# Kernel tuning notes

Measured on AMD Instinct MI355X. Metric: run time of the kernel, lower is better.

## Reference

```python
import jax, jax.numpy as jnp
import numpy as np

ROPE_BASE = 10000.0


def _rope_cos_sin(seq_len, head_dim, dtype=jnp.float32):
    theta = 1.0 / (ROPE_BASE ** (jnp.arange(0, head_dim, 2, dtype=jnp.float32) / head_dim))
    angles = jnp.arange(seq_len, dtype=jnp.float32)[:, None] * theta[None, :]  # [S, hd/2]
    return jnp.cos(angles).astype(dtype), jnp.sin(angles).astype(dtype)


def _apply_rope(x, cos, sin):
    # x: [B, H, S, hd]; cos/sin: [S, hd/2] broadcast over B,H (interleaved pairing)
    x1 = x[..., 0::2]
    x2 = x[..., 1::2]
    c = cos[None, None, :, :]
    s = sin[None, None, :, :]
    y1 = x1 * c - x2 * s
    y2 = x1 * s + x2 * c
    return jnp.stack([y1, y2], axis=-1).reshape(x.shape)


def setup_inputs() -> dict:
    key = jax.random.key(0)
    ks = jax.random.split(key, 5)
    B, S, D = 2, 2048, 1024
    std = 1.0 / np.sqrt(D)
    return {
        "x": jax.random.normal(ks[0], (B, S, D), dtype=jnp.float32),
        "Wq": jax.random.normal(ks[1], (D, D), dtype=jnp.float32) * std,
        "Wk": jax.random.normal(ks[2], (D, D), dtype=jnp.float32) * std,
        "Wv": jax.random.normal(ks[3], (D, D), dtype=jnp.float32) * std,
        "Wo": jax.random.normal(ks[4], (D, D), dtype=jnp.float32) * std,
        "n_heads": 16,
    }


def reference(x, Wq, Wk, Wv, Wo, n_heads):
    B, S, D = x.shape
    H = n_heads
    hd = D // H
    # QKV projections (nn.Linear: x @ W.T), split into heads -> [B, H, S, hd]
    def proj(W):
        return (x @ W.T).reshape(B, S, H, hd).transpose(0, 2, 1, 3)
    q, k, v = proj(Wq), proj(Wk), proj(Wv)
    cos, sin = _rope_cos_sin(S, hd, x.dtype)
    q = _apply_rope(q, cos, sin)
    k = _apply_rope(k, cos, sin)
    # causal scaled dot-product attention
    scale = 1.0 / np.sqrt(hd)
    scores = jnp.einsum('bhqd,bhkd->bhqk', q, k) * scale
    causal = jnp.tril(jnp.ones((S, S), dtype=bool))
    scores = jnp.where(causal[None, None], scores, jnp.finfo(scores.dtype).min)
    attn = jax.nn.softmax(scores, axis=-1)
    out = jnp.einsum('bhqk,bhkd->bhqd', attn, v)  # [B,H,S,hd]
    out = out.transpose(0, 2, 1, 3).reshape(B, S, D)
    return out @ Wo.T
```

## Files before the change

### kernel.cpp

```cpp
#include <hip/hip_runtime.h>
#include <stdint.h>

#define B_  2
#define S_  2048
#define D_  1024
#define H_  16
#define HD_ 64
#define M_  (B_ * S_)
#define XN_ ((size_t)M_ * D_)
#define WN_ ((size_t)D_ * D_)

using bf16x8 = __attribute__((ext_vector_type(8))) short;
using f32x4  = __attribute__((ext_vector_type(4))) float;

__device__ __forceinline__ unsigned short f2bf(float f) {
    union { float f; unsigned u; } v; v.f = f;
    unsigned u = v.u;
    return (unsigned short)((u + 0x7fffu + ((u >> 16) & 1u)) >> 16);
}
__device__ __forceinline__ unsigned short f2bf_trunc(float f) {
    union { float f; unsigned u; } v; v.f = f;
    return (unsigned short)(v.u >> 16);
}
__device__ __forceinline__ float bf2f(unsigned short s) {
    union { unsigned u; float f; } v; v.u = ((unsigned)s) << 16;
    return v.f;
}

__device__ __forceinline__ void gload_lds16(const unsigned short* g, unsigned short* l) {
    __builtin_amdgcn_global_load_lds((const __attribute__((address_space(1))) void*)g,
                                     (__attribute__((address_space(3))) void*)l, 16, 0, 0);
}

__global__ __launch_bounds__(256) void cvt_kernel(
    const float* __restrict__ x,
    const float* __restrict__ Wq, const float* __restrict__ Wk,
    const float* __restrict__ Wv, const float* __restrict__ Wo,
    unsigned short* __restrict__ xb,
    unsigned short* __restrict__ Wqb, unsigned short* __restrict__ Wkb,
    unsigned short* __restrict__ Wvb, unsigned short* __restrict__ Wob)
{
    size_t i = ((size_t)blockIdx.x * 256 + threadIdx.x) * 8;
    const float* src; unsigned short* dst; size_t off;
    if (i < XN_) { src = x; dst = xb; off = i; }
    else {
        size_t j = i - XN_;
        int w = (int)(j >> 20);
        off = j & (WN_ - 1);
        src = (w == 0) ? Wq : (w == 1) ? Wk : (w == 2) ? Wv : Wo;
        dst = (w == 0) ? Wqb : (w == 1) ? Wkb : (w == 2) ? Wvb : Wob;
    }
    float4 a = *(const float4*)(src + off);
    float4 b = *(const float4*)(src + off + 4);
    bf16x8 o;
    o[0] = (short)f2bf(a.x); o[1] = (short)f2bf(a.y);
    o[2] = (short)f2bf(a.z); o[3] = (short)f2bf(a.w);
    o[4] = (short)f2bf(b.x); o[5] = (short)f2bf(b.y);
    o[6] = (short)f2bf(b.z); o[7] = (short)f2bf(b.w);
    *(bf16x8*)(dst + off) = o;
}

__global__ __launch_bounds__(256, 3) void qkv_rope_kernel(
    const unsigned short* __restrict__ x,
    const unsigned short* __restrict__ Wq,
    const unsigned short* __restrict__ Wk,
    const unsigned short* __restrict__ Wv,
    unsigned short* __restrict__ Qo,
    unsigned short* __restrict__ Ko,
    unsigned short* __restrict__ Vt)
{
    __shared__ unsigned short As[128 * 64];
    __shared__ unsigned short Bs[128 * 64];
    const int which = blockIdx.z;
    const unsigned short* __restrict__ W = (which == 0) ? Wq : (which == 1) ? Wk : Wv;
    const int tid  = threadIdx.x;
    const int lane = tid & 63, wave = tid >> 6;
    const int col  = lane & 15, quad = lane >> 4;
    const int wm = (wave >> 1) * 64, wn = (wave & 1) * 64;
    const int n0 = blockIdx.x * 128, m0 = blockIdx.y * 128;
    const int sr = tid >> 3;
    const int sc = tid & 7;
    const int ssw = ((sc ^ (sr & 7)) * 8);

    f32x4 acc[4][4];
#pragma unroll
    for (int i = 0; i < 4; ++i)
#pragma unroll
        for (int j = 0; j < 4; ++j) acc[i][j] = (f32x4){0.f, 0.f, 0.f, 0.f};

    for (int k0 = 0; k0 < D_; k0 += 64) {
        __syncthreads();
#pragma unroll
        for (int g = 0; g < 4; ++g) {
            gload_lds16(x + (size_t)(m0 + g * 32 + sr) * D_ + k0 + ssw, As + g * 2048 + tid * 8);
            gload_lds16(W + (size_t)(n0 + g * 32 + sr) * D_ + k0 + ssw, Bs + g * 2048 + tid * 8);
        }
        __syncthreads();
#pragma unroll
        for (int kk = 0; kk < 2; ++kk) {
            bf16x8 af[4], bf[4];
#pragma unroll
            for (int i = 0; i < 4; ++i) {
                const int R = wm + i * 16 + col;
                af[i] = *(const bf16x8*)&As[R * 64 + (((kk * 4 + quad) ^ (R & 7)) * 8)];
            }
#pragma unroll
            for (int j = 0; j < 4; ++j) {
                const int R = wn + j * 16 + col;
                bf[j] = *(const bf16x8*)&Bs[R * 64 + (((kk * 4 + quad) ^ (R & 7)) * 8)];
            }
#pragma unroll
            for (int i = 0; i < 4; ++i)
#pragma unroll
                for (int j = 0; j < 4; ++j)
                    acc[i][j] = __builtin_amdgcn_mfma_f32_16x16x32_bf16(af[i], bf[j], acc[i][j], 0, 0, 0);
        }
    }

#pragma unroll
    for (int i = 0; i < 4; ++i) {
        const int mg0    = m0 + wm + i * 16 + quad * 4;
        const int bb     = mg0 >> 11;
        const int s_base = mg0 & (S_ - 1);
#pragma unroll
        for (int j = 0; j < 4; ++j) {
            const int n  = n0 + wn + j * 16 + col;
            const int h  = n >> 6;
            const int dd = n & 63;
            if (which < 2) {
                unsigned short* __restrict__ O = (which == 0) ? Qo : Ko;
                const float theta  = __expf(-0.2878231366242557f * (float)(dd >> 1));
                const float qscale = (which == 0) ? 0.125f : 1.0f;
#pragma unroll
                for (int r = 0; r < 4; ++r) {
                    float v  = acc[i][j][r];
                    float vp = __shfl_xor(v, 1);
                    float ang = theta * (float)(s_base + r);
                    float sn, cs; __sincosf(ang, &sn, &cs);
                    float y = (dd & 1) ? (vp * sn + v * cs) : (v * cs - vp * sn);
                    O[((size_t)(bb * H_ + h) * S_ + s_base + r) * HD_ + dd] = f2bf(y * qscale);
                }
            } else {
                ushort4 pk;
                pk.x = f2bf(acc[i][j][0]); pk.y = f2bf(acc[i][j][1]);
                pk.z = f2bf(acc[i][j][2]); pk.w = f2bf(acc[i][j][3]);
                *(ushort4*)(Vt + ((size_t)(bb * H_ + h) * HD_ + dd) * S_ + s_base) = pk;
            }
        }
    }
}

#define PST 72

__global__ __launch_bounds__(256, 3) void attn_kernel(
    const unsigned short* __restrict__ Q,
    const unsigned short* __restrict__ K,
    const unsigned short* __restrict__ Vt,
    unsigned short* __restrict__ num0,
    unsigned short* __restrict__ num1,
    float* __restrict__ den0,
    float* __restrict__ den1)
{
    __shared__ unsigned short KS[64 * 64];
    __shared__ unsigned short VS[64 * 64];
    __shared__ unsigned short Plds[4][16 * PST];
    const int tid  = threadIdx.x;
    const int lane = tid & 63;
    const int wave = tid >> 6;
    const int col  = lane & 15;
    const int quad = lane >> 4;
    const int id = blockIdx.x;
    const int bh = (id & 7) * 4 + ((id >> 3) & 3);
    const int ph = id >> 5;
    const int p  = ph & 7;
    const int hf = ph >> 3;
    const int b = bh >> 4, h = bh & 15;

    unsigned short* __restrict__ nout = hf ? num1 : num0;
    float*          __restrict__ dout = hf ? den1 : den0;

    const unsigned short* Qb = Q  + (size_t)bh * S_ * HD_;
    const unsigned short* Kb = K  + (size_t)bh * S_ * HD_;
    const unsigned short* Vb = Vt + (size_t)bh * HD_ * S_;

    const int srow = tid >> 3;
    const int schk = tid & 7;
    const int ssw0 = (schk ^ (srow & 7)) * 8;

    bf16x8 vone;
#pragma unroll
    for (int e = 0; e < 8; ++e) vone[e] = (short)0x3F80;
    const f32x4 z4 = (f32x4){0.f, 0.f, 0.f, 0.f};
    const float MFIX = 12.0f;

    for (int tt = 0; tt < 2; ++tt) {
        const int t_ = tt ? (15 - p) : p;
        const int q0blk = t_ * 128;
        const int q0w   = q0blk + wave * 32;
        const int nsteps = (q0blk + 128) >> 6;

        bf16x8 aq[2][2];
#pragma unroll
        for (int st = 0; st < 2; ++st) {
            aq[st][0] = *(const bf16x8*)(Qb + (size_t)(q0w + st * 16 + col) * HD_ + quad * 8);
            aq[st][1] = *(const bf16x8*)(Qb + (size_t)(q0w + st * 16 + col) * HD_ + 32 + quad * 8);
        }
        f32x4 acc[2][5];
#pragma unroll
        for (int st = 0; st < 2; ++st)
#pragma unroll
            for (int t = 0; t < 5; ++t) acc[st][t] = (f32x4){0.f, 0.f, 0.f, 0.f};

        for (int s = hf; s < nsteps; s += 2) {
            const int j0 = s << 6;
            __syncthreads();
            gload_lds16(Kb + (size_t)(j0 + srow) * HD_ + ssw0,      KS + tid * 8);
            gload_lds16(Kb + (size_t)(j0 + srow + 32) * HD_ + ssw0, KS + 2048 + tid * 8);
            gload_lds16(Vb + (size_t)srow * S_ + j0 + ssw0,         VS + tid * 8);
            gload_lds16(Vb + (size_t)(srow + 32) * S_ + j0 + ssw0,  VS + 2048 + tid * 8);
            __syncthreads();

            f32x4 sc[2][4];
#pragma unroll
            for (int t2 = 0; t2 < 4; ++t2) {
                const int kr = t2 * 16 + col;
                bf16x8 k0 = *(const bf16x8*)&KS[kr * 64 + ((quad ^ (kr & 7)) * 8)];
                bf16x8 k1 = *(const bf16x8*)&KS[kr * 64 + (((4 + quad) ^ (kr & 7)) * 8)];
                sc[0][t2] = __builtin_amdgcn_mfma_f32_16x16x32_bf16(aq[0][0], k0, z4, 0, 0, 0);
                sc[0][t2] = __builtin_amdgcn_mfma_f32_16x16x32_bf16(aq[0][1], k1, sc[0][t2], 0, 0, 0);
                sc[1][t2] = __builtin_amdgcn_mfma_f32_16x16x32_bf16(aq[1][0], k0, z4, 0, 0, 0);
                sc[1][t2] = __builtin_amdgcn_mfma_f32_16x16x32_bf16(aq[1][1], k1, sc[1][t2], 0, 0, 0);
            }
            bf16x8 vf[8];
#pragma unroll
            for (int t = 0; t < 4; ++t) {
                const int dr = t * 16 + col;
                vf[t * 2]     = *(const bf16x8*)&VS[dr * 64 + ((quad ^ (dr & 7)) * 8)];
                vf[t * 2 + 1] = *(const bf16x8*)&VS[dr * 64 + (((4 + quad) ^ (dr & 7)) * 8)];
            }

#pragma unroll
            for (int st = 0; st < 2; ++st) {
                const bool need_mask = (j0 + 63 > q0w + st * 16);
#pragma unroll
                for (int r = 0; r < 4; ++r) {
                    const int qrow = q0w + st * 16 + quad * 4 + r;
                    float v0 = sc[st][0][r], v1 = sc[st][1][r], v2 = sc[st][2][r], v3 = sc[st][3][r];
                    if (need_mask) {
                        if (j0 + col      > qrow) v0 = -1.0e38f;
                        if (j0 + 16 + col > qrow) v1 = -1.0e38f;
                        if (j0 + 32 + col > qrow) v2 = -1.0e38f;
                        if (j0 + 48 + col > qrow) v3 = -1.0e38f;
                    }
                    const int rb = (quad * 4 + r) * PST;
                    Plds[wave][rb + col]      = f2bf_trunc(__expf(v0 - MFIX));
                    Plds[wave][rb + 16 + col] = f2bf_trunc(__expf(v1 - MFIX));
                    Plds[wave][rb + 32 + col] = f2bf_trunc(__expf(v2 - MFIX));
                    Plds[wave][rb + 48 + col] = f2bf_trunc(__expf(v3 - MFIX));
                }
                bf16x8 ap0 = *(const bf16x8*)&Plds[wave][col * PST + quad * 8];
                bf16x8 ap1 = *(const bf16x8*)&Plds[wave][col * PST + 32 + quad * 8];
#pragma unroll
                for (int t = 0; t < 4; ++t) {
                    acc[st][t] = __builtin_amdgcn_mfma_f32_16x16x32_bf16(ap0, vf[t * 2], acc[st][t], 0, 0, 0);
                    acc[st][t] = __builtin_amdgcn_mfma_f32_16x16x32_bf16(ap1, vf[t * 2 + 1], acc[st][t], 0, 0, 0);
                }
                acc[st][4] = __builtin_amdgcn_mfma_f32_16x16x32_bf16(ap0, vone, acc[st][4], 0, 0, 0);
                acc[st][4] = __builtin_amdgcn_mfma_f32_16x16x32_bf16(ap1, vone, acc[st][4], 0, 0, 0);
            }
        }

#pragma unroll
        for (int st = 0; st < 2; ++st) {
#pragma unroll
            for (int t = 0; t < 4; ++t)
#pragma unroll
                for (int r = 0; r < 4; ++r) {
                    const int qrow = q0w + st * 16 + quad * 4 + r;
                    nout[(size_t)(b * S_ + qrow) * D_ + h * HD_ + t * 16 + col] =
                        f2bf(acc[st][t][r]);
                }
            if (col == 0) {
#pragma unroll
                for (int r = 0; r < 4; ++r) {
                    const int qrow = q0w + st * 16 + quad * 4 + r;
                    dout[(size_t)(b * S_ + qrow) * H_ + h] = acc[st][4][r];
                }
            }
        }
    }
}

__global__ __launch_bounds__(256) void combine_kernel(
    const unsigned short* __restrict__ num0,
    unsigned short* __restrict__ A,
    const float* __restrict__ den0,
    const float* __restrict__ den1)
{
    size_t idx = ((size_t)blockIdx.x * 256 + threadIdx.x) * 8;
    size_t row = idx >> 10;
    int hh = (int)((idx >> 6) & 15);
    float inv = 1.0f / (den0[row * H_ + hh] + den1[row * H_ + hh]);
    bf16x8 a = *(const bf16x8*)(num0 + idx);
    bf16x8 c = *(const bf16x8*)(A + idx);
    bf16x8 o;
#pragma unroll
    for (int e = 0; e < 8; ++e)
        o[e] = (short)f2bf((bf2f((unsigned short)a[e]) + bf2f((unsigned short)c[e])) * inv);
    *(bf16x8*)(A + idx) = o;
}

__global__ __launch_bounds__(256, 3) void oproj_kernel(
    const unsigned short* __restrict__ A,
    const unsigned short* __restrict__ Wo,
    float* __restrict__ out)
{
    __shared__ unsigned short As[128 * 64];
    __shared__ unsigned short Bs[128 * 64];
    const int tid  = threadIdx.x;
    const int lane = tid & 63, wave = tid >> 6;
    const int col  = lane & 15, quad = lane >> 4;
    const int wm = (wave >> 1) * 64, wn = (wave & 1) * 64;
    const int n0 = blockIdx.x * 128, m0 = blockIdx.y * 128;
    const int sr = tid >> 3;
    const int sc = tid & 7;
    const int ssw = ((sc ^ (sr & 7)) * 8);

    f32x4 acc[4][4];
#pragma unroll
    for (int i = 0; i < 4; ++i)
#pragma unroll
        for (int j = 0; j < 4; ++j) acc[i][j] = (f32x4){0.f, 0.f, 0.f, 0.f};

    for (int k0 = 0; k0 < D_; k0 += 64) {
        __syncthreads();
#pragma unroll
        for (int g = 0; g < 4; ++g) {
            gload_lds16(A  + (size_t)(m0 + g * 32 + sr) * D_ + k0 + ssw, As + g * 2048 + tid * 8);
            gload_lds16(Wo + (size_t)(n0 + g * 32 + sr) * D_ + k0 + ssw, Bs + g * 2048 + tid * 8);
        }
        __syncthreads();
#pragma unroll
        for (int kk = 0; kk < 2; ++kk) {
            bf16x8 af[4], bf[4];
#pragma unroll
            for (int i = 0; i < 4; ++i) {
                const int R = wm + i * 16 + col;
                af[i] = *(const bf16x8*)&As[R * 64 + (((kk * 4 + quad) ^ (R & 7)) * 8)];
            }
#pragma unroll
            for (int j = 0; j < 4; ++j) {
                const int R = wn + j * 16 + col;
                bf[j] = *(const bf16x8*)&Bs[R * 64 + (((kk * 4 + quad) ^ (R & 7)) * 8)];
            }
#pragma unroll
            for (int i = 0; i < 4; ++i)
#pragma unroll
                for (int j = 0; j < 4; ++j)
                    acc[i][j] = __builtin_amdgcn_mfma_f32_16x16x32_bf16(af[i], bf[j], acc[i][j], 0, 0, 0);
        }
    }
#pragma unroll
    for (int i = 0; i < 4; ++i) {
        const int mg0 = m0 + wm + i * 16 + quad * 4;
#pragma unroll
        for (int j = 0; j < 4; ++j) {
            const int n = n0 + wn + j * 16 + col;
#pragma unroll
            for (int r = 0; r < 4; ++r)
                out[(size_t)(mg0 + r) * D_ + n] = acc[i][j][r];
        }
    }
}

extern "C" void kernel_launch(void* const* d_in, const int* in_sizes, int n_in,
                              void* d_out, int out_size, void* d_ws, size_t ws_size,
                              hipStream_t stream)
{
    const float* x  = (const float*)d_in[0];
    const float* Wq = (const float*)d_in[1];
    const float* Wk = (const float*)d_in[2];
    const float* Wv = (const float*)d_in[3];
    const float* Wo = (const float*)d_in[4];

    unsigned short* xb  = (unsigned short*)d_ws;
    unsigned short* Wqb = xb  + XN_;
    unsigned short* Wkb = Wqb + WN_;
    unsigned short* Wvb = Wkb + WN_;
    unsigned short* Wob = Wvb + WN_;
    unsigned short* Qw  = Wob + WN_;
    unsigned short* Kw  = Qw  + XN_;
    unsigned short* Vtw = Kw  + XN_;
    unsigned short* Aw  = Vtw + XN_;

    unsigned short* num0 = xb;
    float*          den0 = (float*)Wqb;
    float*          den1 = den0 + (size_t)M_ * H_;

    const int cvt_blocks = (int)((XN_ + 4 * WN_) / (8 * 256));
    cvt_kernel<<<cvt_blocks, 256, 0, stream>>>(x, Wq, Wk, Wv, Wo, xb, Wqb, Wkb, Wvb, Wob);
    qkv_rope_kernel<<<dim3(D_ / 128, M_ / 128, 3), 256, 0, stream>>>(xb, Wqb, Wkb, Wvb, Qw, Kw, Vtw);
    attn_kernel<<<512, 256, 0, stream>>>(Qw, Kw, Vtw, num0, Aw, den0, den1);
    combine_kernel<<<(int)(XN_ / (8 * 256)), 256, 0, stream>>>(num0, Aw, den0, den1);
    oproj_kernel<<<dim3(D_ / 128, M_ / 128), 256, 0, stream>>>(Aw, Wob, (float*)d_out);
}
```

Baseline: 172.6 us.

## Double-buffer LDS tiles in QKV, attention and output projection kernels

Each GEMM kernel and the attention kernel now keeps two LDS buffers and issues the global-to-LDS loads for the next K tile before computing on the current one. This cuts the main loop to one barrier per iteration instead of two. The aim is to hide global load latency behind MFMA work. In exchange the GEMM kernels use twice the LDS, and their launch bounds drop from 3 to 2 blocks per CU.

```diff
diff --git a/kernel.cpp b/kernel.cpp
--- a/kernel.cpp
+++ b/kernel.cpp
@@ -60,7 +60,7 @@
     *(bf16x8*)(dst + off) = o;
 }
 
-__global__ __launch_bounds__(256, 3) void qkv_rope_kernel(
+__global__ __launch_bounds__(256, 2) void qkv_rope_kernel(
     const unsigned short* __restrict__ x,
     const unsigned short* __restrict__ Wq,
     const unsigned short* __restrict__ Wk,
@@ -69,8 +69,8 @@
     unsigned short* __restrict__ Ko,
     unsigned short* __restrict__ Vt)
 {
-    __shared__ unsigned short As[128 * 64];
-    __shared__ unsigned short Bs[128 * 64];
+    __shared__ unsigned short As[2][128 * 64];
+    __shared__ unsigned short Bs[2][128 * 64];
     const int which = blockIdx.z;
     const unsigned short* __restrict__ W = (which == 0) ? Wq : (which == 1) ? Wk : Wv;
     const int tid  = threadIdx.x;
@@ -82,32 +82,38 @@
     const int sc = tid & 7;
     const int ssw = ((sc ^ (sr & 7)) * 8);
 
+    auto stage = [&](int k0, int bsel) {
+#pragma unroll
+        for (int g = 0; g < 4; ++g) {
+            gload_lds16(x + (size_t)(m0 + g * 32 + sr) * D_ + k0 + ssw, &As[bsel][g * 2048 + tid * 8]);
+            gload_lds16(W + (size_t)(n0 + g * 32 + sr) * D_ + k0 + ssw, &Bs[bsel][g * 2048 + tid * 8]);
+        }
+    };
+
     f32x4 acc[4][4];
 #pragma unroll
     for (int i = 0; i < 4; ++i)
 #pragma unroll
         for (int j = 0; j < 4; ++j) acc[i][j] = (f32x4){0.f, 0.f, 0.f, 0.f};
 
-    for (int k0 = 0; k0 < D_; k0 += 64) {
+    stage(0, 0);
+    for (int it = 0; it < 16; ++it) {
         __syncthreads();
-#pragma unroll
-        for (int g = 0; g < 4; ++g) {
-            gload_lds16(x + (size_t)(m0 + g * 32 + sr) * D_ + k0 + ssw, As + g * 2048 + tid * 8);
-            gload_lds16(W + (size_t)(n0 + g * 32 + sr) * D_ + k0 + ssw, Bs + g * 2048 + tid * 8);
-        }
-        __syncthreads();
+        if (it + 1 < 16) stage((it + 1) * 64, (it + 1) & 1);
+        const unsigned short* Ab = &As[it & 1][0];
+        const unsigned short* Bb = &Bs[it & 1][0];
 #pragma unroll
         for (int kk = 0; kk < 2; ++kk) {
             bf16x8 af[4], bf[4];
 #pragma unroll
             for (int i = 0; i < 4; ++i) {
                 const int R = wm + i * 16 + col;
-                af[i] = *(const bf16x8*)&As[R * 64 + (((kk * 4 + quad) ^ (R & 7)) * 8)];
+                af[i] = *(const bf16x8*)&Ab[R * 64 + (((kk * 4 + quad) ^ (R & 7)) * 8)];
             }
 #pragma unroll
             for (int j = 0; j < 4; ++j) {
                 const int R = wn + j * 16 + col;
-                bf[j] = *(const bf16x8*)&Bs[R * 64 + (((kk * 4 + quad) ^ (R & 7)) * 8)];
+                bf[j] = *(const bf16x8*)&Bb[R * 64 + (((kk * 4 + quad) ^ (R & 7)) * 8)];
             }
 #pragma unroll
             for (int i = 0; i < 4; ++i)
@@ -161,8 +167,8 @@
     float* __restrict__ den0,
     float* __restrict__ den1)
 {
-    __shared__ unsigned short KS[64 * 64];
-    __shared__ unsigned short VS[64 * 64];
+    __shared__ unsigned short KS[2][64 * 64];
+    __shared__ unsigned short VS[2][64 * 64];
     __shared__ unsigned short Plds[4][16 * PST];
     const int tid  = threadIdx.x;
     const int lane = tid & 63;
@@ -187,6 +193,13 @@
     const int schk = tid & 7;
     const int ssw0 = (schk ^ (srow & 7)) * 8;
 
+    auto stageKV = [&](int j0, int bsel) {
+        gload_lds16(Kb + (size_t)(j0 + srow) * HD_ + ssw0,      &KS[bsel][tid * 8]);
+        gload_lds16(Kb + (size_t)(j0 + srow + 32) * HD_ + ssw0, &KS[bsel][2048 + tid * 8]);
+        gload_lds16(Vb + (size_t)srow * S_ + j0 + ssw0,         &VS[bsel][tid * 8]);
+        gload_lds16(Vb + (size_t)(srow + 32) * S_ + j0 + ssw0,  &VS[bsel][2048 + tid * 8]);
+    };
+
     bf16x8 vone;
 #pragma unroll
     for (int e = 0; e < 8; ++e) vone[e] = (short)0x3F80;
@@ -197,7 +210,7 @@
         const int t_ = tt ? (15 - p) : p;
         const int q0blk = t_ * 128;
         const int q0w   = q0blk + wave * 32;
-        const int nsteps = (q0blk + 128) >> 6;
+        const int scount = t_ + 1;
 
         bf16x8 aq[2][2];
 #pragma unroll
@@ -211,21 +224,21 @@
 #pragma unroll
             for (int t = 0; t < 5; ++t) acc[st][t] = (f32x4){0.f, 0.f, 0.f, 0.f};
 
-        for (int s = hf; s < nsteps; s += 2) {
-            const int j0 = s << 6;
+        __syncthreads();
+        stageKV(hf << 6, 0);
+        for (int si = 0; si < scount; ++si) {
+            const int j0 = (hf + 2 * si) << 6;
             __syncthreads();
-            gload_lds16(Kb + (size_t)(j0 + srow) * HD_ + ssw0,      KS + tid * 8);
-            gload_lds16(Kb + (size_t)(j0 + srow + 32) * HD_ + ssw0, KS + 2048 + tid * 8);
-            gload_lds16(Vb + (size_t)srow * S_ + j0 + ssw0,         VS + tid * 8);
-            gload_lds16(Vb + (size_t)(srow + 32) * S_ + j0 + ssw0,  VS + 2048 + tid * 8);
-            __syncthreads();
+            if (si + 1 < scount) stageKV((hf + 2 * (si + 1)) << 6, (si + 1) & 1);
+            const unsigned short* KSb = &KS[si & 1][0];
+            const unsigned short* VSb = &VS[si & 1][0];
 
             f32x4 sc[2][4];
 #pragma unroll
             for (int t2 = 0; t2 < 4; ++t2) {
                 const int kr = t2 * 16 + col;
-                bf16x8 k0 = *(const bf16x8*)&KS[kr * 64 + ((quad ^ (kr & 7)) * 8)];
-                bf16x8 k1 = *(const bf16x8*)&KS[kr * 64 + (((4 + quad) ^ (kr & 7)) * 8)];
+                bf16x8 k0 = *(const bf16x8*)&KSb[kr * 64 + ((quad ^ (kr & 7)) * 8)];
+                bf16x8 k1 = *(const bf16x8*)&KSb[kr * 64 + (((4 + quad) ^ (kr & 7)) * 8)];
                 sc[0][t2] = __builtin_amdgcn_mfma_f32_16x16x32_bf16(aq[0][0], k0, z4, 0, 0, 0);
                 sc[0][t2] = __builtin_amdgcn_mfma_f32_16x16x32_bf16(aq[0][1], k1, sc[0][t2], 0, 0, 0);
                 sc[1][t2] = __builtin_amdgcn_mfma_f32_16x16x32_bf16(aq[1][0], k0, z4, 0, 0, 0);
@@ -235,8 +248,8 @@
 #pragma unroll
             for (int t = 0; t < 4; ++t) {
                 const int dr = t * 16 + col;
-                vf[t * 2]     = *(const bf16x8*)&VS[dr * 64 + ((quad ^ (dr & 7)) * 8)];
-                vf[t * 2 + 1] = *(const bf16x8*)&VS[dr * 64 + (((4 + quad) ^ (dr & 7)) * 8)];
+                vf[t * 2]     = *(const bf16x8*)&VSb[dr * 64 + ((quad ^ (dr & 7)) * 8)];
+                vf[t * 2 + 1] = *(const bf16x8*)&VSb[dr * 64 + (((4 + quad) ^ (dr & 7)) * 8)];
             }
 
 #pragma unroll
@@ -310,13 +323,13 @@
     *(bf16x8*)(A + idx) = o;
 }
 
-__global__ __launch_bounds__(256, 3) void oproj_kernel(
+__global__ __launch_bounds__(256, 2) void oproj_kernel(
     const unsigned short* __restrict__ A,
     const unsigned short* __restrict__ Wo,
     float* __restrict__ out)
 {
-    __shared__ unsigned short As[128 * 64];
-    __shared__ unsigned short Bs[128 * 64];
+    __shared__ unsigned short As[2][128 * 64];
+    __shared__ unsigned short Bs[2][128 * 64];
     const int tid  = threadIdx.x;
     const int lane = tid & 63, wave = tid >> 6;
     const int col  = lane & 15, quad = lane >> 4;
@@ -326,32 +339,38 @@
     const int sc = tid & 7;
     const int ssw = ((sc ^ (sr & 7)) * 8);
 
+    auto stage = [&](int k0, int bsel) {
+#pragma unroll
+        for (int g = 0; g < 4; ++g) {
+            gload_lds16(A  + (size_t)(m0 + g * 32 + sr) * D_ + k0 + ssw, &As[bsel][g * 2048 + tid * 8]);
+            gload_lds16(Wo + (size_t)(n0 + g * 32 + sr) * D_ + k0 + ssw, &Bs[bsel][g * 2048 + tid * 8]);
+        }
+    };
+
     f32x4 acc[4][4];
 #pragma unroll
     for (int i = 0; i < 4; ++i)
 #pragma unroll
         for (int j = 0; j < 4; ++j) acc[i][j] = (f32x4){0.f, 0.f, 0.f, 0.f};
 
-    for (int k0 = 0; k0 < D_; k0 += 64) {
+    stage(0, 0);
+    for (int it = 0; it < 16; ++it) {
         __syncthreads();
-#pragma unroll
-        for (int g = 0; g < 4; ++g) {
-            gload_lds16(A  + (size_t)(m0 + g * 32 + sr) * D_ + k0 + ssw, As + g * 2048 + tid * 8);
-            gload_lds16(Wo + (size_t)(n0 + g * 32 + sr) * D_ + k0 + ssw, Bs + g * 2048 + tid * 8);
-        }
-        __syncthreads();
+        if (it + 1 < 16) stage((it + 1) * 64, (it + 1) & 1);
+        const unsigned short* Ab = &As[it & 1][0];
+        const unsigned short* Bb = &Bs[it & 1][0];
 #pragma unroll
         for (int kk = 0; kk < 2; ++kk) {
             bf16x8 af[4], bf[4];
 #pragma unroll
             for (int i = 0; i < 4; ++i) {
                 const int R = wm + i * 16 + col;
-                af[i] = *(const bf16x8*)&As[R * 64 + (((kk * 4 + quad) ^ (R & 7)) * 8)];
+                af[i] = *(const bf16x8*)&Ab[R * 64 + (((kk * 4 + quad) ^ (R & 7)) * 8)];
             }
 #pragma unroll
             for (int j = 0; j < 4; ++j) {
                 const int R = wn + j * 16 + col;
-                bf[j] = *(const bf16x8*)&Bs[R * 64 + (((kk * 4 + quad) ^ (R & 7)) * 8)];
+                bf[j] = *(const bf16x8*)&Bb[R * 64 + (((kk * 4 + quad) ^ (R & 7)) * 8)];
             }
 #pragma unroll
             for (int i = 0; i < 4; ++i)
```

Result: slower. 186.4 us (+8.0%).

## Double-buffer LDS tiles with BK=32 in QKV and output projection GEMMs

Applied to the files above, without the earlier changes.

Both projection GEMM kernels switch from a single 64-wide K tile with two barriers per step to two 32-wide K buffers in LDS. The next tile is prefetched into the other buffer while MFMAs run on the current one, using one barrier per iteration and a swizzle adjusted for 32-wide rows. The aim is to hide global-to-LDS load latency behind compute. The cost is twice as many loop iterations with half the MFMA work each. Correctness also depends on the async LDS loads having completed by the single barrier.

```diff
diff --git a/kernel.cpp b/kernel.cpp
--- a/kernel.cpp
+++ b/kernel.cpp
@@ -69,8 +69,8 @@
     unsigned short* __restrict__ Ko,
     unsigned short* __restrict__ Vt)
 {
-    __shared__ unsigned short As[128 * 64];
-    __shared__ unsigned short Bs[128 * 64];
+    __shared__ unsigned short As[2][128 * 32];
+    __shared__ unsigned short Bs[2][128 * 32];
     const int which = blockIdx.z;
     const unsigned short* __restrict__ W = (which == 0) ? Wq : (which == 1) ? Wk : Wv;
     const int tid  = threadIdx.x;
@@ -78,9 +78,17 @@
     const int col  = lane & 15, quad = lane >> 4;
     const int wm = (wave >> 1) * 64, wn = (wave & 1) * 64;
     const int n0 = blockIdx.x * 128, m0 = blockIdx.y * 128;
-    const int sr = tid >> 3;
-    const int sc = tid & 7;
-    const int ssw = ((sc ^ (sr & 7)) * 8);
+    const int sr = tid >> 2;
+    const int sc = tid & 3;
+    const int ssw = ((sc ^ (sr & 3)) * 8);
+
+    auto stage = [&](int k0, int bsel) {
+#pragma unroll
+        for (int g = 0; g < 2; ++g) {
+            gload_lds16(x + (size_t)(m0 + g * 64 + sr) * D_ + k0 + ssw, &As[bsel][g * 2048 + tid * 8]);
+            gload_lds16(W + (size_t)(n0 + g * 64 + sr) * D_ + k0 + ssw, &Bs[bsel][g * 2048 + tid * 8]);
+        }
+    };
 
     f32x4 acc[4][4];
 #pragma unroll
@@ -88,33 +96,28 @@
 #pragma unroll
         for (int j = 0; j < 4; ++j) acc[i][j] = (f32x4){0.f, 0.f, 0.f, 0.f};
 
-    for (int k0 = 0; k0 < D_; k0 += 64) {
+    stage(0, 0);
+    for (int it = 0; it < 32; ++it) {
         __syncthreads();
-#pragma unroll
-        for (int g = 0; g < 4; ++g) {
-            gload_lds16(x + (size_t)(m0 + g * 32 + sr) * D_ + k0 + ssw, As + g * 2048 + tid * 8);
-            gload_lds16(W + (size_t)(n0 + g * 32 + sr) * D_ + k0 + ssw, Bs + g * 2048 + tid * 8);
-        }
-        __syncthreads();
-#pragma unroll
-        for (int kk = 0; kk < 2; ++kk) {
-            bf16x8 af[4], bf[4];
-#pragma unroll
-            for (int i = 0; i < 4; ++i) {
-                const int R = wm + i * 16 + col;
-                af[i] = *(const bf16x8*)&As[R * 64 + (((kk * 4 + quad) ^ (R & 7)) * 8)];
-            }
-#pragma unroll
-            for (int j = 0; j < 4; ++j) {
-                const int R = wn + j * 16 + col;
-                bf[j] = *(const bf16x8*)&Bs[R * 64 + (((kk * 4 + quad) ^ (R & 7)) * 8)];
-            }
-#pragma unroll
-            for (int i = 0; i < 4; ++i)
-#pragma unroll
-                for (int j = 0; j < 4; ++j)
-                    acc[i][j] = __builtin_amdgcn_mfma_f32_16x16x32_bf16(af[i], bf[j], acc[i][j], 0, 0, 0);
-        }
+        if (it + 1 < 32) stage((it + 1) * 32, (it + 1) & 1);
+        const unsigned short* Ab = &As[it & 1][0];
+        const unsigned short* Bb = &Bs[it & 1][0];
+        bf16x8 af[4], bf[4];
+#pragma unroll
+        for (int i = 0; i < 4; ++i) {
+            const int R = wm + i * 16 + col;
+            af[i] = *(const bf16x8*)&Ab[R * 32 + ((quad ^ (R & 3)) * 8)];
+        }
+#pragma unroll
+        for (int j = 0; j < 4; ++j) {
+            const int R = wn + j * 16 + col;
+            bf[j] = *(const bf16x8*)&Bb[R * 32 + ((quad ^ (R & 3)) * 8)];
+        }
+#pragma unroll
+        for (int i = 0; i < 4; ++i)
+#pragma unroll
+            for (int j = 0; j < 4; ++j)
+                acc[i][j] = __builtin_amdgcn_mfma_f32_16x16x32_bf16(af[i], bf[j], acc[i][j], 0, 0, 0);
     }
 
 #pragma unroll
@@ -315,16 +318,24 @@
     const unsigned short* __restrict__ Wo,
     float* __restrict__ out)
 {
-    __shared__ unsigned short As[128 * 64];
-    __shared__ unsigned short Bs[128 * 64];
+    __shared__ unsigned short As[2][128 * 32];
+    __shared__ unsigned short Bs[2][128 * 32];
     const int tid  = threadIdx.x;
     const int lane = tid & 63, wave = tid >> 6;
     const int col  = lane & 15, quad = lane >> 4;
     const int wm = (wave >> 1) * 64, wn = (wave & 1) * 64;
     const int n0 = blockIdx.x * 128, m0 = blockIdx.y * 128;
-    const int sr = tid >> 3;
-    const int sc = tid & 7;
-    const int ssw = ((sc ^ (sr & 7)) * 8);
+    const int sr = tid >> 2;
+    const int sc = tid & 3;
+    const int ssw = ((sc ^ (sr & 3)) * 8);
+
+    auto stage = [&](int k0, int bsel) {
+#pragma unroll
+        for (int g = 0; g < 2; ++g) {
+            gload_lds16(A  + (size_t)(m0 + g * 64 + sr) * D_ + k0 + ssw, &As[bsel][g * 2048 + tid * 8]);
+            gload_lds16(Wo + (size_t)(n0 + g * 64 + sr) * D_ + k0 + ssw, &Bs[bsel][g * 2048 + tid * 8]);
+        }
+    };
 
     f32x4 acc[4][4];
 #pragma unroll
@@ -332,33 +343,28 @@
 #pragma unroll
         for (int j = 0; j < 4; ++j) acc[i][j] = (f32x4){0.f, 0.f, 0.f, 0.f};
 
-    for (int k0 = 0; k0 < D_; k0 += 64) {
+    stage(0, 0);
+    for (int it = 0; it < 32; ++it) {
         __syncthreads();
-#pragma unroll
-        for (int g = 0; g < 4; ++g) {
-            gload_lds16(A  + (size_t)(m0 + g * 32 + sr) * D_ + k0 + ssw, As + g * 2048 + tid * 8);
-            gload_lds16(Wo + (size_t)(n0 + g * 32 + sr) * D_ + k0 + ssw, Bs + g * 2048 + tid * 8);
-        }
-        __syncthreads();
-#pragma unroll
-        for (int kk = 0; kk < 2; ++kk) {
-            bf16x8 af[4], bf[4];
-#pragma unroll
-            for (int i = 0; i < 4; ++i) {
-                const int R = wm + i * 16 + col;
-                af[i] = *(const bf16x8*)&As[R * 64 + (((kk * 4 + quad) ^ (R & 7)) * 8)];
-            }
-#pragma unroll
-            for (int j = 0; j < 4; ++j) {
-                const int R = wn + j * 16 + col;
-                bf[j] = *(const bf16x8*)&Bs[R * 64 + (((kk * 4 + quad) ^ (R & 7)) * 8)];
-            }
-#pragma unroll
-            for (int i = 0; i < 4; ++i)
-#pragma unroll
-                for (int j = 0; j < 4; ++j)
-                    acc[i][j] = __builtin_amdgcn_mfma_f32_16x16x32_bf16(af[i], bf[j], acc[i][j], 0, 0, 0);
-        }
+        if (it + 1 < 32) stage((it + 1) * 32, (it + 1) & 1);
+        const unsigned short* Ab = &As[it & 1][0];
+        const unsigned short* Bb = &Bs[it & 1][0];
+        bf16x8 af[4], bf[4];
+#pragma unroll
+        for (int i = 0; i < 4; ++i) {
+            const int R = wm + i * 16 + col;
+            af[i] = *(const bf16x8*)&Ab[R * 32 + ((quad ^ (R & 3)) * 8)];
+        }
+#pragma unroll
+        for (int j = 0; j < 4; ++j) {
+            const int R = wn + j * 16 + col;
+            bf[j] = *(const bf16x8*)&Bb[R * 32 + ((quad ^ (R & 3)) * 8)];
+        }
+#pragma unroll
+        for (int i = 0; i < 4; ++i)
+#pragma unroll
+            for (int j = 0; j < 4; ++j)
+                acc[i][j] = __builtin_amdgcn_mfma_f32_16x16x32_bf16(af[i], bf[j], acc[i][j], 0, 0, 0);
     }
 #pragma unroll
     for (int i = 0; i < 4; ++i) {
```

Measured after the change: 181.1 us. 1.05x slower.

## Transpose attention MFMA operands to pack P writes and fold softmax constants

Applied to the files above, without the earlier changes.

Swaps the operand order of the QK^T and PV MFMAs so each lane holds four consecutive key scores for a single query. That lets the probability tile be written to LDS as one packed 8-byte store per tile instead of many scalar 2-byte stores, and lets the numerator be written to global memory as packed ushort4 stores. The log2(e) factor is folded into the Q scale and the fixed max offset into the MFMA accumulator init, so the softmax uses exp2f with no per-element subtract. The masking index math changes to match the transposed layout, and the denominator path stays in the original layout; getting either wrong would change results.

```diff
diff --git a/kernel.cpp b/kernel.cpp
--- a/kernel.cpp
+++ b/kernel.cpp
@@ -18,13 +18,12 @@
     unsigned u = v.u;
     return (unsigned short)((u + 0x7fffu + ((u >> 16) & 1u)) >> 16);
 }
-__device__ __forceinline__ unsigned short f2bf_trunc(float f) {
-    union { float f; unsigned u; } v; v.f = f;
-    return (unsigned short)(v.u >> 16);
-}
 __device__ __forceinline__ float bf2f(unsigned short s) {
     union { unsigned u; float f; } v; v.u = ((unsigned)s) << 16;
     return v.f;
+}
+__device__ __forceinline__ unsigned fbits(float f) {
+    union { float f; unsigned u; } v; v.f = f; return v.u;
 }
 
 __device__ __forceinline__ void gload_lds16(const unsigned short* g, unsigned short* l) {
@@ -130,7 +129,7 @@
             if (which < 2) {
                 unsigned short* __restrict__ O = (which == 0) ? Qo : Ko;
                 const float theta  = __expf(-0.2878231366242557f * (float)(dd >> 1));
-                const float qscale = (which == 0) ? 0.125f : 1.0f;
+                const float qscale = (which == 0) ? 0.18033688f : 1.0f;
 #pragma unroll
                 for (int r = 0; r < 4; ++r) {
                     float v  = acc[i][j][r];
@@ -151,6 +150,7 @@
 }
 
 #define PST 72
+#define MFIX2 17.312340490667561f
 
 __global__ __launch_bounds__(256, 3) void attn_kernel(
     const unsigned short* __restrict__ Q,
@@ -190,8 +190,7 @@
     bf16x8 vone;
 #pragma unroll
     for (int e = 0; e < 8; ++e) vone[e] = (short)0x3F80;
-    const f32x4 z4 = (f32x4){0.f, 0.f, 0.f, 0.f};
-    const float MFIX = 12.0f;
+    const f32x4 mfixv = (f32x4){-MFIX2, -MFIX2, -MFIX2, -MFIX2};
 
     for (int tt = 0; tt < 2; ++tt) {
         const int t_ = tt ? (15 - p) : p;
@@ -220,16 +219,16 @@
             gload_lds16(Vb + (size_t)(srow + 32) * S_ + j0 + ssw0,  VS + 2048 + tid * 8);
             __syncthreads();
 
-            f32x4 sc[2][4];
+            f32x4 scT[2][4];
 #pragma unroll
             for (int t2 = 0; t2 < 4; ++t2) {
                 const int kr = t2 * 16 + col;
                 bf16x8 k0 = *(const bf16x8*)&KS[kr * 64 + ((quad ^ (kr & 7)) * 8)];
                 bf16x8 k1 = *(const bf16x8*)&KS[kr * 64 + (((4 + quad) ^ (kr & 7)) * 8)];
-                sc[0][t2] = __builtin_amdgcn_mfma_f32_16x16x32_bf16(aq[0][0], k0, z4, 0, 0, 0);
-                sc[0][t2] = __builtin_amdgcn_mfma_f32_16x16x32_bf16(aq[0][1], k1, sc[0][t2], 0, 0, 0);
-                sc[1][t2] = __builtin_amdgcn_mfma_f32_16x16x32_bf16(aq[1][0], k0, z4, 0, 0, 0);
-                sc[1][t2] = __builtin_amdgcn_mfma_f32_16x16x32_bf16(aq[1][1], k1, sc[1][t2], 0, 0, 0);
+                scT[0][t2] = __builtin_amdgcn_mfma_f32_16x16x32_bf16(k0, aq[0][0], mfixv, 0, 0, 0);
+                scT[0][t2] = __builtin_amdgcn_mfma_f32_16x16x32_bf16(k1, aq[0][1], scT[0][t2], 0, 0, 0);
+                scT[1][t2] = __builtin_amdgcn_mfma_f32_16x16x32_bf16(k0, aq[1][0], mfixv, 0, 0, 0);
+                scT[1][t2] = __builtin_amdgcn_mfma_f32_16x16x32_bf16(k1, aq[1][1], scT[1][t2], 0, 0, 0);
             }
             bf16x8 vf[8];
 #pragma unroll
@@ -242,28 +241,26 @@
 #pragma unroll
             for (int st = 0; st < 2; ++st) {
                 const bool need_mask = (j0 + 63 > q0w + st * 16);
-#pragma unroll
-                for (int r = 0; r < 4; ++r) {
-                    const int qrow = q0w + st * 16 + quad * 4 + r;
-                    float v0 = sc[st][0][r], v1 = sc[st][1][r], v2 = sc[st][2][r], v3 = sc[st][3][r];
-                    if (need_mask) {
-                        if (j0 + col      > qrow) v0 = -1.0e38f;
-                        if (j0 + 16 + col > qrow) v1 = -1.0e38f;
-                        if (j0 + 32 + col > qrow) v2 = -1.0e38f;
-                        if (j0 + 48 + col > qrow) v3 = -1.0e38f;
+                const int  qrow = q0w + st * 16 + col;
+#pragma unroll
+                for (int t2 = 0; t2 < 4; ++t2) {
+                    float pv[4];
+#pragma unroll
+                    for (int r = 0; r < 4; ++r) {
+                        float sv = scT[st][t2][r];
+                        if (need_mask && (j0 + t2 * 16 + quad * 4 + r > qrow)) sv = -1.0e38f;
+                        pv[r] = exp2f(sv);
                     }
-                    const int rb = (quad * 4 + r) * PST;
-                    Plds[wave][rb + col]      = f2bf_trunc(__expf(v0 - MFIX));
-                    Plds[wave][rb + 16 + col] = f2bf_trunc(__expf(v1 - MFIX));
-                    Plds[wave][rb + 32 + col] = f2bf_trunc(__expf(v2 - MFIX));
-                    Plds[wave][rb + 48 + col] = f2bf_trunc(__expf(v3 - MFIX));
+                    unsigned lo = (fbits(pv[0]) >> 16) | (fbits(pv[1]) & 0xffff0000u);
+                    unsigned hi = (fbits(pv[2]) >> 16) | (fbits(pv[3]) & 0xffff0000u);
+                    *(uint2*)&Plds[wave][col * PST + t2 * 16 + quad * 4] = (uint2){lo, hi};
                 }
                 bf16x8 ap0 = *(const bf16x8*)&Plds[wave][col * PST + quad * 8];
                 bf16x8 ap1 = *(const bf16x8*)&Plds[wave][col * PST + 32 + quad * 8];
 #pragma unroll
                 for (int t = 0; t < 4; ++t) {
-                    acc[st][t] = __builtin_amdgcn_mfma_f32_16x16x32_bf16(ap0, vf[t * 2], acc[st][t], 0, 0, 0);
-                    acc[st][t] = __builtin_amdgcn_mfma_f32_16x16x32_bf16(ap1, vf[t * 2 + 1], acc[st][t], 0, 0, 0);
+                    acc[st][t] = __builtin_amdgcn_mfma_f32_16x16x32_bf16(vf[t * 2], ap0, acc[st][t], 0, 0, 0);
+                    acc[st][t] = __builtin_amdgcn_mfma_f32_16x16x32_bf16(vf[t * 2 + 1], ap1, acc[st][t], 0, 0, 0);
                 }
                 acc[st][4] = __builtin_amdgcn_mfma_f32_16x16x32_bf16(ap0, vone, acc[st][4], 0, 0, 0);
                 acc[st][4] = __builtin_amdgcn_mfma_f32_16x16x32_bf16(ap1, vone, acc[st][4], 0, 0, 0);
@@ -272,20 +269,18 @@
 
 #pragma unroll
         for (int st = 0; st < 2; ++st) {
-#pragma unroll
-            for (int t = 0; t < 4; ++t)
-#pragma unroll
-                for (int r = 0; r < 4; ++r) {
-                    const int qrow = q0w + st * 16 + quad * 4 + r;
-                    nout[(size_t)(b * S_ + qrow) * D_ + h * HD_ + t * 16 + col] =
-                        f2bf(acc[st][t][r]);
-                }
+            const int qrow = q0w + st * 16 + col;
+#pragma unroll
+            for (int t = 0; t < 4; ++t) {
+                ushort4 pk;
+                pk.x = f2bf(acc[st][t][0]); pk.y = f2bf(acc[st][t][1]);
+                pk.z = f2bf(acc[st][t][2]); pk.w = f2bf(acc[st][t][3]);
+                *(ushort4*)&nout[(size_t)(b * S_ + qrow) * D_ + h * HD_ + t * 16 + quad * 4] = pk;
+            }
             if (col == 0) {
 #pragma unroll
-                for (int r = 0; r < 4; ++r) {
-                    const int qrow = q0w + st * 16 + quad * 4 + r;
-                    dout[(size_t)(b * S_ + qrow) * H_ + h] = acc[st][4][r];
-                }
+                for (int r = 0; r < 4; ++r)
+                    dout[(size_t)(b * S_ + q0w + st * 16 + quad * 4 + r) * H_ + h] = acc[st][4][r];
             }
         }
     }
```

New measurement: 184.6 us. 1.07x slower.
